# Kernel optimization log

Hardware: AMD Instinct MI355X
Metric: run time of the kernel (lower is better)

## Reference

```python
import jax, jax.numpy as jnp
import numpy as np

# Complete 4-ary tree, leaves at depth 8, heap layout (children of i are 4i+1..4i+4).
B_ARY = 4
DEPTH = 8          # depths 0..8, leaves at depth 8
H = 512            # hidden_channels
IN = 512           # in_channels
OUT = 256          # out_channels
L = 2              # num_layers
LEVEL_STARTS = np.array([(B_ARY ** d - 1) // (B_ARY - 1) for d in range(DEPTH + 2)])
N = int(LEVEL_STARTS[-1])  # 87381


def setup_inputs() -> dict:
    key = jax.random.key(0)
    ks = jax.random.split(key, 12)
    x = jax.random.normal(ks[0], (N, IN), jnp.float32)

    # tree structure (numpy, deterministic)
    n_internal = int(LEVEL_STARTS[DEPTH])
    child_idx = np.zeros((N, B_ARY), np.int32)
    child_mask = np.zeros((N, B_ARY), np.int32)
    internal = np.arange(n_internal)
    child_idx[:n_internal] = (internal[:, None] * B_ARY + 1 + np.arange(B_ARY)[None, :]).astype(np.int32)
    child_mask[:n_internal] = 1
    node_parent = np.full(N, -1, np.int64)
    node_parent[1:] = (np.arange(1, N) - 1) // B_ARY
    node_depth = np.zeros(N, np.int64)
    for d in range(DEPTH + 1):
        node_depth[LEVEL_STARTS[d]:LEVEL_STARTS[d + 1]] = d
    is_leaf = node_depth == DEPTH
    edge_index = np.stack([np.arange(1, N), node_parent[1:]]).astype(np.int64)
    batch = np.zeros(N, np.int64)

    s = 0.02
    params = dict(
        W_in=jax.random.normal(ks[1], (IN, H), jnp.float32) * s,
        b_in=jnp.zeros((H,), jnp.float32),
        W_ioux=jax.random.normal(ks[2], (L, H, 3 * H), jnp.float32) * s,
        b_ioux=jnp.zeros((L, 3 * H), jnp.float32),
        W_iouh=jax.random.normal(ks[3], (L, H, 3 * H), jnp.float32) * s,
        b_iouh=jnp.zeros((L, 3 * H), jnp.float32),
        W_fx=jax.random.normal(ks[4], (L, H, H), jnp.float32) * s,
        b_fx=jnp.zeros((L, H), jnp.float32),
        W_fh=jax.random.normal(ks[5], (L, H, H), jnp.float32) * s,
        b_fh=jnp.zeros((L, H), jnp.float32),
        W_out=jax.random.normal(ks[6], (H, OUT), jnp.float32) * s,
        b_out=jnp.zeros((OUT,), jnp.float32),
    )
    return dict(
        x=x,
        edge_index=jnp.asarray(edge_index),
        batch=jnp.asarray(batch),
        node_depth=jnp.asarray(node_depth),
        node_parent=jnp.asarray(node_parent),
        is_leaf=jnp.asarray(is_leaf),
        child_idx=jnp.asarray(child_idx),
        child_mask=jnp.asarray(child_mask),
        **params,
    )


def reference(x, edge_index, batch, node_depth, node_parent, is_leaf,
              child_idx, child_mask,
              W_in, b_in, W_ioux, b_ioux, W_iouh, b_iouh,
              W_fx, b_fx, W_fh, b_fh, W_out, b_out):
    cm = child_mask.astype(x.dtype)  # [N, B]
    h = jax.nn.relu(x @ W_in + b_in)  # input projection (dropout = eval mode identity)
    for l in range(L):
        hidden = jnp.zeros((N, H), x.dtype)
        cell = jnp.zeros((N, H), x.dtype)
        # bottom-up over tree levels; levels are contiguous static slices
        for d in range(DEPTH, -1, -1):
            s, e = int(LEVEL_STARTS[d]), int(LEVEL_STARTS[d + 1])
            xl = h[s:e]                                   # [n_d, H]
            ci = child_idx[s:e]                           # [n_d, B]
            m = cm[s:e][..., None]                        # [n_d, B, 1]
            ch = hidden[ci] * m                           # masked child hidden
            cc = cell[ci] * m                             # masked child cell
            h_sum = ch.sum(axis=1)                        # child-sum
            iou = xl @ W_ioux[l] + b_ioux[l] + h_sum @ W_iouh[l] + b_iouh[l]
            i, o, u = jnp.split(iou, 3, axis=-1)
            i = jax.nn.sigmoid(i)
            o = jax.nn.sigmoid(o)
            u = jnp.tanh(u)
            f = jax.nn.sigmoid((xl @ W_fx[l] + b_fx[l])[:, None, :] + ch @ W_fh[l] + b_fh[l])
            c = i * u + (f * cc).sum(axis=1)
            hl = o * jnp.tanh(c)
            hidden = hidden.at[s:e].set(hl)
            cell = cell.at[s:e].set(c)
        h = hidden
    node_emb = h @ W_out + b_out                          # [N, OUT]
    tree_emb = jax.ops.segment_sum(node_emb, batch, num_segments=1)  # 'sum' aggregation
    return node_emb, tree_emb
```

## Files before the change

### kernel.cpp

```cpp
#include <hip/hip_runtime.h>

typedef __bf16 bf16;
typedef __bf16 bf16x8 __attribute__((ext_vector_type(8)));
typedef float f32x4 __attribute__((ext_vector_type(4)));

#define NN 87381
#define NINT 21845
#define NLEAF 65536
#define LEAF_START 21845

__device__ __forceinline__ float sigmoidf_(float x) {
    return 1.0f / (1.0f + __expf(-x));
}
__device__ __forceinline__ float tanhf_(float x) {
    return 1.0f - 2.0f / (__expf(2.0f * x) + 1.0f);
}

__device__ __forceinline__ void gload_lds16(const bf16* g, bf16* l) {
    __builtin_amdgcn_global_load_lds(
        (const __attribute__((address_space(1))) unsigned int*)g,
        (__attribute__((address_space(3))) unsigned int*)l, 16, 0, 0);
}

__device__ __forceinline__ int xcd_swz(int bid, int nwg) {
    int q = nwg >> 3, r = nwg & 7;
    int x = bid & 7, i = bid >> 3;
    return (x < r ? x * (q + 1) : r * (q + 1) + (x - r) * q) + i;
}

#define SWZ(r, kc) ((((r) << 3) | ((kc) ^ ((r) & 7))) << 3)

__global__ void tconv_kernel(const float* __restrict__ W, bf16* __restrict__ Wt,
                             int NR, int total) {
    int idx = blockIdx.x * 256 + threadIdx.x;
    if (idx >= total) return;
    int n = idx >> 9;
    int k = idx & 511;
    Wt[idx] = (bf16)W[(size_t)k * NR + n];
}

__global__ void tcat_kernel(const float* __restrict__ W1, const float* __restrict__ W2,
                            bf16* __restrict__ Wt, int NR, int total) {
    int idx = blockIdx.x * 256 + threadIdx.x;
    if (idx >= total) return;
    int n = idx >> 10;
    int kk = idx & 1023;
    const float* src = (kk < 512) ? W1 : W2;
    int k = kk & 511;
    Wt[idx] = (bf16)src[(size_t)k * NR + n];
}

__global__ void convx_kernel(const float* __restrict__ X, bf16* __restrict__ Y, int total4) {
    int idx = blockIdx.x * 256 + threadIdx.x;
    if (idx >= total4) return;
    const float4 f = *reinterpret_cast<const float4*>(X + (size_t)idx * 4);
    bf16 o[4] = {(bf16)f.x, (bf16)f.y, (bf16)f.z, (bf16)f.w};
    *reinterpret_cast<ushort2*>(Y + (size_t)idx * 4 + 0) = *reinterpret_cast<ushort2*>(&o[0]);
    *reinterpret_cast<ushort2*>(Y + (size_t)idx * 4 + 2) = *reinterpret_cast<ushort2*>(&o[2]);
}

#define MFMA_COMPUTE_2x4(As, Bs, acc, wm, wn, lm, quad)                          \
    _Pragma("unroll")                                                            \
    for (int kk = 0; kk < 64; kk += 32) {                                        \
        const int kc_ = (kk >> 3) + quad;                                        \
        bf16x8 areg[2], breg[4];                                                 \
        _Pragma("unroll")                                                        \
        for (int mi = 0; mi < 2; ++mi)                                           \
            areg[mi] = *reinterpret_cast<const bf16x8*>(                         \
                &(As)[SWZ(wm + mi * 16 + lm, kc_)]);                             \
        _Pragma("unroll")                                                        \
        for (int ni = 0; ni < 4; ++ni)                                           \
            breg[ni] = *reinterpret_cast<const bf16x8*>(                         \
                &(Bs)[SWZ(wn + ni * 16 + lm, kc_)]);                             \
        _Pragma("unroll")                                                        \
        for (int mi = 0; mi < 2; ++mi)                                           \
            _Pragma("unroll")                                                    \
            for (int ni = 0; ni < 4; ++ni)                                       \
                acc[mi][ni] = __builtin_amdgcn_mfma_f32_16x16x32_bf16(           \
                    areg[mi], breg[ni], acc[mi][ni], 0, 0, 0);                   \
    }

__global__ __launch_bounds__(512)
void gemm_kernel(const bf16* __restrict__ A, const bf16* __restrict__ Bt,
                 int bstride, int K, int ntiles,
                 float* __restrict__ Cf, bf16* __restrict__ Cb,
                 const float* __restrict__ bias1, const float* __restrict__ bias2,
                 int M, int N, int relu, int swz)
{
    __shared__ __align__(16) bf16 As[2][128 * 64];
    __shared__ __align__(16) bf16 Bs[2][128 * 64];
    const int tid  = threadIdx.x;
    const int wave = tid >> 6;
    const int lane = tid & 63;
    int bid = blockIdx.x;
    if (swz) bid = xcd_swz(bid, (int)gridDim.x);
    const int bm = (bid / ntiles) * 128;
    const int bn = (bid % ntiles) * 128;
    const int wm = (wave & 3) * 32;
    const int wn = (wave >> 2) * 64;
    const int lm   = lane & 15;
    const int quad = lane >> 4;

    f32x4 acc[2][4];
#pragma unroll
    for (int i = 0; i < 2; ++i)
#pragma unroll
        for (int j = 0; j < 4; ++j) acc[i][j] = (f32x4){0.f, 0.f, 0.f, 0.f};

    const bf16* aptr[2];
    const bf16* bptr[2];
    int loff[2];
#pragma unroll
    for (int i = 0; i < 2; ++i) {
        int c   = i * 512 + tid;
        int r   = c >> 3;
        int kc8 = ((c & 7) ^ (r & 7)) << 3;
        int gr  = bm + r; gr = (gr < M) ? gr : (M - 1);
        aptr[i] = A + (size_t)gr * K + kc8;
        bptr[i] = Bt + (size_t)(bn + r) * bstride + kc8;
        loff[i] = c << 3;
    }

    auto stage = [&](int buf, int t) {
        const int kofs = t << 6;
#pragma unroll
        for (int i = 0; i < 2; ++i)
            gload_lds16(aptr[i] + kofs, &As[0][0] + buf * (128 * 64) + loff[i]);
#pragma unroll
        for (int i = 0; i < 2; ++i)
            gload_lds16(bptr[i] + kofs, &Bs[0][0] + buf * (128 * 64) + loff[i]);
    };

    const int nk = K >> 6;
    stage(0, 0);
    __syncthreads();
    int cur = 0;
    for (int t = 0; t < nk; ++t) {
        if (t + 1 < nk) stage(cur ^ 1, t + 1);
        MFMA_COMPUTE_2x4(As[cur], Bs[cur], acc, wm, wn, lm, quad);
        __syncthreads();
        cur ^= 1;
    }

#pragma unroll
    for (int ni = 0; ni < 4; ++ni) {
        int col = bn + wn + ni * 16 + lm;
        float bsum = (bias1 ? bias1[col] : 0.f) + (bias2 ? bias2[col] : 0.f);
#pragma unroll
        for (int mi = 0; mi < 2; ++mi) {
#pragma unroll
            for (int r = 0; r < 4; ++r) {
                int row = bm + wm + mi * 16 + quad * 4 + r;
                if (row < M) {
                    float v = acc[mi][ni][r] + bsum;
                    if (relu) v = (v > 0.f) ? v : 0.f;
                    if (Cf) Cf[(size_t)row * N + col] = v;
                    else    Cb[(size_t)row * N + col] = (bf16)v;
                }
            }
        }
    }
}

__global__ __launch_bounds__(512)
void iou_fused_kernel(const bf16* __restrict__ A0, const bf16* __restrict__ A1,
                      int K, const bf16* __restrict__ wiou,
                      const float* __restrict__ bx1, const float* __restrict__ bx2,
                      const float* __restrict__ fcs,
                      bf16* __restrict__ hout, bf16* __restrict__ cellout,
                      bf16* __restrict__ hsout,
                      int M, int swz)
{
    __shared__ __align__(16) bf16 As[2][128 * 64];
    __shared__ __align__(16) bf16 Bs[2][3 * 64 * 64];
    const int tid  = threadIdx.x;
    const int wave = tid >> 6;
    const int lane = tid & 63;
    int bid = blockIdx.x;
    if (swz) bid = xcd_swz(bid, (int)gridDim.x);
    const int bm = (bid >> 3) * 128;
    const int bn = (bid & 7) * 64;
    if (bm >= M) return;
    const int wm   = (wave & 3) * 32;
    const int wn   = (wave >> 2) * 32;
    const int lm   = lane & 15;
    const int quad = lane >> 4;

    f32x4 acc[3][2][2];
#pragma unroll
    for (int g = 0; g < 3; ++g)
#pragma unroll
        for (int i = 0; i < 2; ++i)
#pragma unroll
            for (int j = 0; j < 2; ++j) acc[g][i][j] = (f32x4){0.f, 0.f, 0.f, 0.f};

    const bf16* A1s = A1 ? A1 : A0;
    const bf16* aptr0[2];
    const bf16* aptr1[2];
    int aoff[2];
#pragma unroll
    for (int i = 0; i < 2; ++i) {
        int c   = i * 512 + tid;
        int r   = c >> 3;
        int kc8 = ((c & 7) ^ (r & 7)) << 3;
        int gr  = bm + r; gr = (gr < M) ? gr : (M - 1);
        aptr0[i] = A0  + ((size_t)gr << 9) + kc8;
        aptr1[i] = A1s + ((size_t)gr << 9) + kc8;
        aoff[i]  = c << 3;
    }
    const bf16* bptr[3];
    int boff[3];
#pragma unroll
    for (int i = 0; i < 3; ++i) {
        int c   = i * 512 + tid;
        int g   = c >> 9;
        int cg  = c & 511;
        int r   = cg >> 3;
        int kc8 = ((cg & 7) ^ (r & 7)) << 3;
        bptr[i] = wiou + (size_t)(g * 512 + bn + r) * 1024 + kc8;
        boff[i] = c << 3;
    }

    auto stage = [&](int buf, int t) {
        const int kofs = (t & 7) << 6;
#pragma unroll
        for (int i = 0; i < 2; ++i) {
            const bf16* g = ((t < 8) ? aptr0[i] : aptr1[i]) + kofs;
            gload_lds16(g, &As[0][0] + buf * (128 * 64) + aoff[i]);
        }
        const int bofs = t << 6;
#pragma unroll
        for (int i = 0; i < 3; ++i)
            gload_lds16(bptr[i] + bofs, &Bs[0][0] + buf * (3 * 64 * 64) + boff[i]);
    };

    const int nk = K >> 6;
    stage(0, 0);
    __syncthreads();
    int cur = 0;
    for (int t = 0; t < nk; ++t) {
        if (t + 1 < nk) stage(cur ^ 1, t + 1);
#pragma unroll
        for (int kk = 0; kk < 64; kk += 32) {
            const int kc_ = (kk >> 3) + quad;
            bf16x8 areg[2];
#pragma unroll
            for (int mi = 0; mi < 2; ++mi)
                areg[mi] = *reinterpret_cast<const bf16x8*>(
                    &As[cur][SWZ(wm + mi * 16 + lm, kc_)]);
            bf16x8 breg[3][2];
#pragma unroll
            for (int g = 0; g < 3; ++g)
#pragma unroll
                for (int ni = 0; ni < 2; ++ni)
                    breg[g][ni] = *reinterpret_cast<const bf16x8*>(
                        &Bs[cur][g * 4096 + SWZ(wn + ni * 16 + lm, kc_)]);
#pragma unroll
            for (int g = 0; g < 3; ++g)
#pragma unroll
                for (int mi = 0; mi < 2; ++mi)
#pragma unroll
                    for (int ni = 0; ni < 2; ++ni)
                        acc[g][mi][ni] = __builtin_amdgcn_mfma_f32_16x16x32_bf16(
                            areg[mi], breg[g][ni], acc[g][mi][ni], 0, 0, 0);
        }
        __syncthreads();
        cur ^= 1;
    }

#pragma unroll
    for (int ni = 0; ni < 2; ++ni) {
        int col = bn + wn + ni * 16 + lm;
        float bi = bx1[col]        + bx2[col];
        float bo = bx1[col + 512]  + bx2[col + 512];
        float bu = bx1[col + 1024] + bx2[col + 1024];
#pragma unroll
        for (int mi = 0; mi < 2; ++mi) {
            int rbase = bm + wm + mi * 16 + quad * 4;
            float hsum = 0.f;
#pragma unroll
            for (int r = 0; r < 4; ++r) {
                int row = rbase + r;
                if (row < M) {
                    float i_ = sigmoidf_(acc[0][mi][ni][r] + bi);
                    float o_ = sigmoidf_(acc[1][mi][ni][r] + bo);
                    float u_ = tanhf_(acc[2][mi][ni][r] + bu);
                    float c  = i_ * u_ + (fcs ? fcs[(size_t)row * 512 + col] : 0.f);
                    bf16 hb  = (bf16)(o_ * tanhf_(c));
                    cellout[(size_t)row * 512 + col] = (bf16)c;
                    hout[(size_t)row * 512 + col] = hb;
                    hsum += (float)hb;
                }
            }
            if (hsout && rbase < M)
                hsout[(size_t)(rbase >> 2) * 512 + col] = (bf16)hsum;
        }
    }
}

__global__ __launch_bounds__(512)
void cf_kernel(const bf16* __restrict__ hp, const bf16* __restrict__ hc,
               const bf16* __restrict__ cellc, const bf16* __restrict__ wf,
               const float* __restrict__ bf1, const float* __restrict__ bf2,
               float* __restrict__ fcs, int E, int swz)
{
    const int M = 4 * E;
    __shared__ __align__(16) bf16 As[2][128 * 64];
    __shared__ __align__(16) bf16 Bs[2][128 * 64];
    const int tid  = threadIdx.x;
    const int wave = tid >> 6;
    const int lane = tid & 63;
    int bid = blockIdx.x;
    if (swz) bid = xcd_swz(bid, (int)gridDim.x);
    const int bm = (bid >> 2) * 128;
    const int bn = (bid & 3) * 128;
    if (bm >= M) return;
    const int wm   = (wave & 3) * 32;
    const int wn   = (wave >> 2) * 64;
    const int lm   = lane & 15;
    const int quad = lane >> 4;

    f32x4 acc[2][4];
#pragma unroll
    for (int i = 0; i < 2; ++i)
#pragma unroll
        for (int j = 0; j < 4; ++j) acc[i][j] = (f32x4){0.f, 0.f, 0.f, 0.f};

    const bf16* aptrP[2];
    const bf16* aptrC[2];
    const bf16* bptr[2];
    int loff[2];
#pragma unroll
    for (int i = 0; i < 2; ++i) {
        int c   = i * 512 + tid;
        int r   = c >> 3;
        int kc8 = ((c & 7) ^ (r & 7)) << 3;
        int gr  = bm + r; gr = (gr < M) ? gr : (M - 1);
        aptrP[i] = hp + ((size_t)(gr >> 2) << 9) + kc8;
        aptrC[i] = hc + ((size_t)gr << 9) + kc8;
        bptr[i]  = wf + (size_t)(bn + r) * 1024 + kc8;
        loff[i]  = c << 3;
    }

    auto stage = [&](int buf, int t) {
        const int kofs = (t & 7) << 6;
#pragma unroll
        for (int i = 0; i < 2; ++i) {
            const bf16* g = ((t < 8) ? aptrP[i] : aptrC[i]) + kofs;
            gload_lds16(g, &As[0][0] + buf * (128 * 64) + loff[i]);
        }
        const int bofs = t << 6;
#pragma unroll
        for (int i = 0; i < 2; ++i)
            gload_lds16(bptr[i] + bofs, &Bs[0][0] + buf * (128 * 64) + loff[i]);
    };

    stage(0, 0);
    __syncthreads();
    int cur = 0;
    for (int t = 0; t < 16; ++t) {
        if (t + 1 < 16) stage(cur ^ 1, t + 1);
        MFMA_COMPUTE_2x4(As[cur], Bs[cur], acc, wm, wn, lm, quad);
        __syncthreads();
        cur ^= 1;
    }

#pragma unroll
    for (int ni = 0; ni < 4; ++ni) {
        int col = bn + wn + ni * 16 + lm;
        float bsum = bf1[col] + bf2[col];
#pragma unroll
        for (int mi = 0; mi < 2; ++mi) {
            int R0 = bm + wm + mi * 16;
            if (R0 + quad * 4 < M) {
                float fc = 0.f;
#pragma unroll
                for (int r = 0; r < 4; ++r) {
                    int row = R0 + quad * 4 + r;
                    fc += sigmoidf_(acc[mi][ni][r] + bsum) *
                          (float)cellc[(size_t)row * 512 + col];
                }
                fcs[(size_t)((R0 >> 2) + quad) * 512 + col] = fc;
            }
        }
    }
}

#define R1_BLOCKS 2048
#define R1_ROWS 43
__global__ void reduce1_kernel(const float* __restrict__ ne, float* __restrict__ partial)
{
    int t = threadIdx.x;
    int b = blockIdx.x;
    int r0 = b * R1_ROWS;
    int r1 = r0 + R1_ROWS; r1 = (r1 < NN) ? r1 : NN;
    float acc = 0.f;
    for (int r = r0; r < r1; ++r) acc += ne[(size_t)r * 256 + t];
    partial[(size_t)b * 256 + t] = acc;
}
__global__ void reduce2_kernel(const float* __restrict__ partial, float* __restrict__ partial2)
{
    int t = threadIdx.x;
    int b = blockIdx.x;
    float acc = 0.f;
    for (int i = 0; i < 32; ++i) acc += partial[(size_t)(b * 32 + i) * 256 + t];
    partial2[(size_t)b * 256 + t] = acc;
}
__global__ void reduce3_kernel(const float* __restrict__ partial2, float* __restrict__ tree)
{
    int t = threadIdx.x;
    float acc = 0.f;
    for (int i = 0; i < 64; ++i) acc += partial2[(size_t)i * 256 + t];
    tree[t] = acc;
}

extern "C" void kernel_launch(void* const* d_in, const int* in_sizes, int n_in,
                              void* d_out, int out_size, void* d_ws, size_t ws_size,
                              hipStream_t stream)
{
    const float* x      = (const float*)d_in[0];
    const float* W_in   = (const float*)d_in[8];
    const float* b_in   = (const float*)d_in[9];
    const float* W_ioux = (const float*)d_in[10];
    const float* b_ioux = (const float*)d_in[11];
    const float* W_iouh = (const float*)d_in[12];
    const float* b_iouh = (const float*)d_in[13];
    const float* W_fx   = (const float*)d_in[14];
    const float* b_fx   = (const float*)d_in[15];
    const float* W_fh   = (const float*)d_in[16];
    const float* b_fh   = (const float*)d_in[17];
    const float* W_out  = (const float*)d_in[18];
    const float* b_out  = (const float*)d_in[19];

    static const int LS[10] = {0, 1, 5, 21, 85, 341, 1365, 5461, 21845, 87381};

    char* ws = (char*)d_ws;
    size_t off = 0;
    auto take = [&](size_t bytes) -> void* {
        void* p = ws + off;
        off += (bytes + 255) & ~(size_t)255;
        return p;
    };
    bf16*  wt_in      = (bf16*) take((size_t)512 * 512 * 2);
    bf16*  wt_out     = (bf16*) take((size_t)256 * 512 * 2);
    bf16*  wt_iou_cat = (bf16*) take((size_t)2 * 1536 * 1024 * 2);
    bf16*  wt_f_cat   = (bf16*) take((size_t)2 * 512 * 1024 * 2);
    bf16*  h          = (bf16*) take((size_t)NN * 512 * 2);
    bf16*  hint1      = (bf16*) take((size_t)NINT * 512 * 2);
    bf16*  hB         = (bf16*) take((size_t)NLEAF * 512 * 2);
    bf16*  cell_int   = (bf16*) take((size_t)NINT * 512 * 2);
    bf16*  cell_leaf  = (bf16*) take((size_t)NLEAF * 512 * 2);
    float* fcsum      = (float*)take((size_t)16384 * 512 * 4);
    bf16*  hsA        = (bf16*) take((size_t)16384 * 512 * 2);
    bf16*  hsB        = (bf16*) take((size_t)4096 * 512 * 2);
    float* partial    = (float*)take((size_t)R1_BLOCKS * 256 * 4);
    float* partial2   = (float*)take((size_t)64 * 256 * 4);
    bf16*  xbf        = cell_int;

    dim3 blk(256), blk512(512);
    auto tgrid = [](int total) { return dim3((unsigned)((total + 255) / 256)); };

    tconv_kernel<<<tgrid(512 * 512), blk, 0, stream>>>(W_in, wt_in, 512, 512 * 512);
    tconv_kernel<<<tgrid(256 * 512), blk, 0, stream>>>(W_out, wt_out, 256, 256 * 512);
    for (int l = 0; l < 2; ++l) {
        tcat_kernel<<<tgrid(1536 * 1024), blk, 0, stream>>>(
            W_ioux + (size_t)l * 512 * 1536, W_iouh + (size_t)l * 512 * 1536,
            wt_iou_cat + (size_t)l * 1536 * 1024, 1536, 1536 * 1024);
        tcat_kernel<<<tgrid(512 * 1024), blk, 0, stream>>>(
            W_fx + (size_t)l * 512 * 512, W_fh + (size_t)l * 512 * 512,
            wt_f_cat + (size_t)l * 512 * 1024, 512, 512 * 1024);
    }

    auto gemm = [&](const bf16* A, const bf16* Bt, int bstride, int K,
                    float* Cf, bf16* Cb, const float* b1, const float* b2,
                    int M, int N, int relu, int swz) {
        int mt = (M + 127) / 128, nt = N / 128;
        gemm_kernel<<<dim3((unsigned)(mt * nt)), blk512, 0, stream>>>(
            A, Bt, bstride, K, nt, Cf, Cb, b1, b2, M, N, relu, swz);
    };

    convx_kernel<<<tgrid(NN * 128), blk, 0, stream>>>(x, xbf, NN * 128);
    gemm(xbf, wt_in, 512, 512, nullptr, h, b_in, nullptr, NN, 512, 1, 1);

    for (int l = 0; l < 2; ++l) {
        const bf16* wiou = wt_iou_cat + (size_t)l * 1536 * 1024;
        const bf16* wf   = wt_f_cat + (size_t)l * 512 * 1024;
        const float* bx1 = b_ioux + (size_t)l * 1536;
        const float* bx2 = b_iouh + (size_t)l * 1536;
        const float* bf1 = b_fx + (size_t)l * 512;
        const float* bf2 = b_fh + (size_t)l * 512;

        const bf16* lin   = (l == 0) ? (h + (size_t)LEAF_START * 512) : hB;
        bf16*       lout  = (l == 0) ? hB : (h + (size_t)LEAF_START * 512);
        const bf16* hprev = (l == 0) ? h : hint1;
        bf16*       hcur  = (l == 0) ? hint1 : h;

        {
            int mt = NLEAF / 128;
            iou_fused_kernel<<<dim3((unsigned)(mt * 8)), blk512, 0, stream>>>(
                lin, nullptr, 512, wiou, bx1, bx2, nullptr,
                lout, cell_leaf, hsA, NLEAF, 1);
        }

        for (int d = 7; d >= 0; --d) {
            int s  = LS[d];
            int E  = LS[d + 1] - LS[d];
            int cs = LS[d + 1];
            const bf16* hc = (d == 7) ? lout : (hcur + (size_t)cs * 512);
            const bf16* cc = (d == 7) ? cell_leaf : (cell_int + (size_t)cs * 512);
            bf16* hs_read  = (d & 1) ? hsA : hsB;
            bf16* hs_write = (d == 0) ? nullptr : ((d & 1) ? hsB : hsA);

            int mt_cf = (4 * E + 127) / 128;
            cf_kernel<<<dim3((unsigned)(mt_cf * 4)), blk512, 0, stream>>>(
                hprev + (size_t)s * 512, hc, cc, wf, bf1, bf2, fcsum, E, 1);

            int mt_iou = (E + 127) / 128;
            iou_fused_kernel<<<dim3((unsigned)(mt_iou * 8)), blk512, 0, stream>>>(
                hprev + (size_t)s * 512, hs_read, 1024, wiou, bx1, bx2, fcsum,
                hcur + (size_t)s * 512, cell_int + (size_t)s * 512, hs_write, E, 1);
        }
    }

    float* node_emb = (float*)d_out;
    gemm(h, wt_out, 512, 512, node_emb, nullptr, b_out, nullptr, NN, 256, 0, 1);
    reduce1_kernel<<<dim3(R1_BLOCKS), blk, 0, stream>>>(node_emb, partial);
    reduce2_kernel<<<dim3(64), blk, 0, stream>>>(partial, partial2);
    reduce3_kernel<<<dim3(1), blk, 0, stream>>>(partial2, node_emb + (size_t)NN * 256);
}
```

Before: 1.717 ms.

## Precompute input projections for all internal nodes in one batched GEMM per layer

The x-dependent terms (xl@W_ioux and xl@W_fx) for all internal nodes are now computed up front in one large GEMM into a bf16 XOUT buffer, instead of being recomputed inside each per-level iou and forget-gate kernel with a concatenated K=1024. The per-level kernels then run with K=512 and add the precomputed terms in their epilogues. The cf kernel previously multiplied each parent's row four times (once per child). This removes that redundant work and shortens the serial per-level chain. In exchange it adds an extra GEMM, a bf16 round-trip of the pre-activations, and more weight-conversion launches.

```diff
diff --git a/kernel.cpp b/kernel.cpp
--- a/kernel.cpp
+++ b/kernel.cpp
@@ -37,17 +37,6 @@
     int n = idx >> 9;
     int k = idx & 511;
     Wt[idx] = (bf16)W[(size_t)k * NR + n];
-}
-
-__global__ void tcat_kernel(const float* __restrict__ W1, const float* __restrict__ W2,
-                            bf16* __restrict__ Wt, int NR, int total) {
-    int idx = blockIdx.x * 256 + threadIdx.x;
-    if (idx >= total) return;
-    int n = idx >> 10;
-    int kk = idx & 1023;
-    const float* src = (kk < 512) ? W1 : W2;
-    int k = kk & 511;
-    Wt[idx] = (bf16)src[(size_t)k * NR + n];
 }
 
 __global__ void convx_kernel(const float* __restrict__ X, bf16* __restrict__ Y, int total4) {
@@ -163,10 +152,9 @@
 }
 
 __global__ __launch_bounds__(512)
-void iou_fused_kernel(const bf16* __restrict__ A0, const bf16* __restrict__ A1,
-                      int K, const bf16* __restrict__ wiou,
+void iou_fused_kernel(const bf16* __restrict__ A, const bf16* __restrict__ wiou,
                       const float* __restrict__ bx1, const float* __restrict__ bx2,
-                      const float* __restrict__ fcs,
+                      const float* __restrict__ fcs, const bf16* __restrict__ xout,
                       bf16* __restrict__ hout, bf16* __restrict__ cellout,
                       bf16* __restrict__ hsout,
                       int M, int swz)
@@ -194,9 +182,7 @@
 #pragma unroll
             for (int j = 0; j < 2; ++j) acc[g][i][j] = (f32x4){0.f, 0.f, 0.f, 0.f};
 
-    const bf16* A1s = A1 ? A1 : A0;
-    const bf16* aptr0[2];
-    const bf16* aptr1[2];
+    const bf16* aptr[2];
     int aoff[2];
 #pragma unroll
     for (int i = 0; i < 2; ++i) {
@@ -204,9 +190,8 @@
         int r   = c >> 3;
         int kc8 = ((c & 7) ^ (r & 7)) << 3;
         int gr  = bm + r; gr = (gr < M) ? gr : (M - 1);
-        aptr0[i] = A0  + ((size_t)gr << 9) + kc8;
-        aptr1[i] = A1s + ((size_t)gr << 9) + kc8;
-        aoff[i]  = c << 3;
+        aptr[i] = A + ((size_t)gr << 9) + kc8;
+        aoff[i] = c << 3;
     }
     const bf16* bptr[3];
     int boff[3];
@@ -217,29 +202,25 @@
         int cg  = c & 511;
         int r   = cg >> 3;
         int kc8 = ((cg & 7) ^ (r & 7)) << 3;
-        bptr[i] = wiou + (size_t)(g * 512 + bn + r) * 1024 + kc8;
+        bptr[i] = wiou + (size_t)(g * 512 + bn + r) * 512 + kc8;
         boff[i] = c << 3;
     }
 
     auto stage = [&](int buf, int t) {
-        const int kofs = (t & 7) << 6;
-#pragma unroll
-        for (int i = 0; i < 2; ++i) {
-            const bf16* g = ((t < 8) ? aptr0[i] : aptr1[i]) + kofs;
-            gload_lds16(g, &As[0][0] + buf * (128 * 64) + aoff[i]);
-        }
-        const int bofs = t << 6;
+        const int kofs = t << 6;
+#pragma unroll
+        for (int i = 0; i < 2; ++i)
+            gload_lds16(aptr[i] + kofs, &As[0][0] + buf * (128 * 64) + aoff[i]);
 #pragma unroll
         for (int i = 0; i < 3; ++i)
-            gload_lds16(bptr[i] + bofs, &Bs[0][0] + buf * (3 * 64 * 64) + boff[i]);
+            gload_lds16(bptr[i] + kofs, &Bs[0][0] + buf * (3 * 64 * 64) + boff[i]);
     };
 
-    const int nk = K >> 6;
     stage(0, 0);
     __syncthreads();
     int cur = 0;
-    for (int t = 0; t < nk; ++t) {
-        if (t + 1 < nk) stage(cur ^ 1, t + 1);
+    for (int t = 0; t < 8; ++t) {
+        if (t + 1 < 8) stage(cur ^ 1, t + 1);
 #pragma unroll
         for (int kk = 0; kk < 64; kk += 32) {
             const int kc_ = (kk >> 3) + quad;
@@ -282,9 +263,15 @@
             for (int r = 0; r < 4; ++r) {
                 int row = rbase + r;
                 if (row < M) {
-                    float i_ = sigmoidf_(acc[0][mi][ni][r] + bi);
-                    float o_ = sigmoidf_(acc[1][mi][ni][r] + bo);
-                    float u_ = tanhf_(acc[2][mi][ni][r] + bu);
+                    float ax = 0.f, aox = 0.f, aux = 0.f;
+                    if (xout) {
+                        ax  = (float)xout[(size_t)row * 2048 + col];
+                        aox = (float)xout[(size_t)row * 2048 + 512 + col];
+                        aux = (float)xout[(size_t)row * 2048 + 1024 + col];
+                    }
+                    float i_ = sigmoidf_(acc[0][mi][ni][r] + ax + bi);
+                    float o_ = sigmoidf_(acc[1][mi][ni][r] + aox + bo);
+                    float u_ = tanhf_(acc[2][mi][ni][r] + aux + bu);
                     float c  = i_ * u_ + (fcs ? fcs[(size_t)row * 512 + col] : 0.f);
                     bf16 hb  = (bf16)(o_ * tanhf_(c));
                     cellout[(size_t)row * 512 + col] = (bf16)c;
@@ -299,8 +286,8 @@
 }
 
 __global__ __launch_bounds__(512)
-void cf_kernel(const bf16* __restrict__ hp, const bf16* __restrict__ hc,
-               const bf16* __restrict__ cellc, const bf16* __restrict__ wf,
+void cf_kernel(const bf16* __restrict__ hc, const bf16* __restrict__ cellc,
+               const bf16* __restrict__ wfh, const bf16* __restrict__ xout,
                const float* __restrict__ bf1, const float* __restrict__ bf2,
                float* __restrict__ fcs, int E, int swz)
 {
@@ -326,8 +313,7 @@
 #pragma unroll
         for (int j = 0; j < 4; ++j) acc[i][j] = (f32x4){0.f, 0.f, 0.f, 0.f};
 
-    const bf16* aptrP[2];
-    const bf16* aptrC[2];
+    const bf16* aptr[2];
     const bf16* bptr[2];
     int loff[2];
 #pragma unroll
@@ -336,30 +322,26 @@
         int r   = c >> 3;
         int kc8 = ((c & 7) ^ (r & 7)) << 3;
         int gr  = bm + r; gr = (gr < M) ? gr : (M - 1);
-        aptrP[i] = hp + ((size_t)(gr >> 2) << 9) + kc8;
-        aptrC[i] = hc + ((size_t)gr << 9) + kc8;
-        bptr[i]  = wf + (size_t)(bn + r) * 1024 + kc8;
-        loff[i]  = c << 3;
+        aptr[i] = hc + ((size_t)gr << 9) + kc8;
+        bptr[i] = wfh + (size_t)(bn + r) * 512 + kc8;
+        loff[i] = c << 3;
     }
 
     auto stage = [&](int buf, int t) {
-        const int kofs = (t & 7) << 6;
-#pragma unroll
-        for (int i = 0; i < 2; ++i) {
-            const bf16* g = ((t < 8) ? aptrP[i] : aptrC[i]) + kofs;
-            gload_lds16(g, &As[0][0] + buf * (128 * 64) + loff[i]);
-        }
-        const int bofs = t << 6;
+        const int kofs = t << 6;
 #pragma unroll
         for (int i = 0; i < 2; ++i)
-            gload_lds16(bptr[i] + bofs, &Bs[0][0] + buf * (128 * 64) + loff[i]);
+            gload_lds16(aptr[i] + kofs, &As[0][0] + buf * (128 * 64) + loff[i]);
+#pragma unroll
+        for (int i = 0; i < 2; ++i)
+            gload_lds16(bptr[i] + kofs, &Bs[0][0] + buf * (128 * 64) + loff[i]);
     };
 
     stage(0, 0);
     __syncthreads();
     int cur = 0;
-    for (int t = 0; t < 16; ++t) {
-        if (t + 1 < 16) stage(cur ^ 1, t + 1);
+    for (int t = 0; t < 8; ++t) {
+        if (t + 1 < 8) stage(cur ^ 1, t + 1);
         MFMA_COMPUTE_2x4(As[cur], Bs[cur], acc, wm, wn, lm, quad);
         __syncthreads();
         cur ^= 1;
@@ -373,14 +355,16 @@
         for (int mi = 0; mi < 2; ++mi) {
             int R0 = bm + wm + mi * 16;
             if (R0 + quad * 4 < M) {
+                int p = (R0 >> 2) + quad;
+                float pf = (float)xout[(size_t)p * 2048 + 1536 + col] + bsum;
                 float fc = 0.f;
 #pragma unroll
                 for (int r = 0; r < 4; ++r) {
                     int row = R0 + quad * 4 + r;
-                    fc += sigmoidf_(acc[mi][ni][r] + bsum) *
+                    fc += sigmoidf_(acc[mi][ni][r] + pf) *
                           (float)cellc[(size_t)row * 512 + col];
                 }
-                fcs[(size_t)((R0 >> 2) + quad) * 512 + col] = fc;
+                fcs[(size_t)p * 512 + col] = fc;
             }
         }
     }
@@ -443,8 +427,9 @@
     };
     bf16*  wt_in      = (bf16*) take((size_t)512 * 512 * 2);
     bf16*  wt_out     = (bf16*) take((size_t)256 * 512 * 2);
-    bf16*  wt_iou_cat = (bf16*) take((size_t)2 * 1536 * 1024 * 2);
-    bf16*  wt_f_cat   = (bf16*) take((size_t)2 * 512 * 1024 * 2);
+    bf16*  wt_xcat    = (bf16*) take((size_t)2 * 2048 * 512 * 2);
+    bf16*  wt_iouh    = (bf16*) take((size_t)2 * 1536 * 512 * 2);
+    bf16*  wt_fh      = (bf16*) take((size_t)2 * 512 * 512 * 2);
     bf16*  h          = (bf16*) take((size_t)NN * 512 * 2);
     bf16*  hint1      = (bf16*) take((size_t)NINT * 512 * 2);
     bf16*  hB         = (bf16*) take((size_t)NLEAF * 512 * 2);
@@ -453,6 +438,7 @@
     float* fcsum      = (float*)take((size_t)16384 * 512 * 4);
     bf16*  hsA        = (bf16*) take((size_t)16384 * 512 * 2);
     bf16*  hsB        = (bf16*) take((size_t)4096 * 512 * 2);
+    bf16*  XOUT       = (bf16*) take((size_t)NINT * 2048 * 2);
     float* partial    = (float*)take((size_t)R1_BLOCKS * 256 * 4);
     float* partial2   = (float*)take((size_t)64 * 256 * 4);
     bf16*  xbf        = cell_int;
@@ -463,12 +449,17 @@
     tconv_kernel<<<tgrid(512 * 512), blk, 0, stream>>>(W_in, wt_in, 512, 512 * 512);
     tconv_kernel<<<tgrid(256 * 512), blk, 0, stream>>>(W_out, wt_out, 256, 256 * 512);
     for (int l = 0; l < 2; ++l) {
-        tcat_kernel<<<tgrid(1536 * 1024), blk, 0, stream>>>(
-            W_ioux + (size_t)l * 512 * 1536, W_iouh + (size_t)l * 512 * 1536,
-            wt_iou_cat + (size_t)l * 1536 * 1024, 1536, 1536 * 1024);
-        tcat_kernel<<<tgrid(512 * 1024), blk, 0, stream>>>(
-            W_fx + (size_t)l * 512 * 512, W_fh + (size_t)l * 512 * 512,
-            wt_f_cat + (size_t)l * 512 * 1024, 512, 512 * 1024);
+        bf16* xc = wt_xcat + (size_t)l * 2048 * 512;
+        tconv_kernel<<<tgrid(1536 * 512), blk, 0, stream>>>(
+            W_ioux + (size_t)l * 512 * 1536, xc, 1536, 1536 * 512);
+        tconv_kernel<<<tgrid(512 * 512), blk, 0, stream>>>(
+            W_fx + (size_t)l * 512 * 512, xc + (size_t)1536 * 512, 512, 512 * 512);
+        tconv_kernel<<<tgrid(1536 * 512), blk, 0, stream>>>(
+            W_iouh + (size_t)l * 512 * 1536, wt_iouh + (size_t)l * 1536 * 512,
+            1536, 1536 * 512);
+        tconv_kernel<<<tgrid(512 * 512), blk, 0, stream>>>(
+            W_fh + (size_t)l * 512 * 512, wt_fh + (size_t)l * 512 * 512,
+            512, 512 * 512);
     }
 
     auto gemm = [&](const bf16* A, const bf16* Bt, int bstride, int K,
@@ -483,8 +474,9 @@
     gemm(xbf, wt_in, 512, 512, nullptr, h, b_in, nullptr, NN, 512, 1, 1);
 
     for (int l = 0; l < 2; ++l) {
-        const bf16* wiou = wt_iou_cat + (size_t)l * 1536 * 1024;
-        const bf16* wf   = wt_f_cat + (size_t)l * 512 * 1024;
+        const bf16* wxc  = wt_xcat + (size_t)l * 2048 * 512;
+        const bf16* wih  = wt_iouh + (size_t)l * 1536 * 512;
+        const bf16* wfh  = wt_fh + (size_t)l * 512 * 512;
         const float* bx1 = b_ioux + (size_t)l * 1536;
         const float* bx2 = b_iouh + (size_t)l * 1536;
         const float* bf1 = b_fx + (size_t)l * 512;
@@ -495,11 +487,14 @@
         const bf16* hprev = (l == 0) ? h : hint1;
         bf16*       hcur  = (l == 0) ? hint1 : h;
 
+        gemm(hprev, wxc, 512, 512, nullptr, XOUT, nullptr, nullptr,
+             NINT, 2048, 0, 1);
+
         {
             int mt = NLEAF / 128;
             iou_fused_kernel<<<dim3((unsigned)(mt * 8)), blk512, 0, stream>>>(
-                lin, nullptr, 512, wiou, bx1, bx2, nullptr,
-                lout, cell_leaf, hsA, NLEAF, 1);
+                lin, wxc , bx1, bx2,
+                nullptr, nullptr, lout, cell_leaf, hsA, NLEAF, 1);
         }
 
         for (int d = 7; d >= 0; --d) {
@@ -510,14 +505,15 @@
             const bf16* cc = (d == 7) ? cell_leaf : (cell_int + (size_t)cs * 512);
             bf16* hs_read  = (d & 1) ? hsA : hsB;
             bf16* hs_write = (d == 0) ? nullptr : ((d & 1) ? hsB : hsA);
+            const bf16* xo = XOUT + (size_t)s * 2048;
 
             int mt_cf = (4 * E + 127) / 128;
             cf_kernel<<<dim3((unsigned)(mt_cf * 4)), blk512, 0, stream>>>(
-                hprev + (size_t)s * 512, hc, cc, wf, bf1, bf2, fcsum, E, 1);
+                hc, cc, wfh, xo, bf1, bf2, fcsum, E, 1);
 
             int mt_iou = (E + 127) / 128;
             iou_fused_kernel<<<dim3((unsigned)(mt_iou * 8)), blk512, 0, stream>>>(
-                hprev + (size_t)s * 512, hs_read, 1024, wiou, bx1, bx2, fcsum,
+                hs_read, wih, bx1, bx2, fcsum, xo,
                 hcur + (size_t)s * 512, cell_int + (size_t)s * 512, hs_write, E, 1);
         }
     }
```

Result: no change. 1.720 ms (+0.2%).
